# Optimization experiments

Hardware: AMD Instinct MI355X
Metric: run time of the kernel (lower is better)

Reference implementation:

```python
import jax, jax.numpy as jnp
import numpy as np

N_NODES = 20000
N_EDGES = 160000
IN_DIM = 64
HID = 256
EDGE_DIM = 64
SF_DIM = 1  # node_counts_dim = max_cycle - MIN_CYCLE + 1 with MIN_CYCLE==max_cycle (source bug)
N_LAYERS = 3
NUM_GRAPHS = 128
MSG_IN = 2 * HID + 2 * SF_DIM + EDGE_DIM  # 578
UPD_IN = 2 * HID


def setup_inputs() -> dict:
    key = jax.random.key(0)
    ks = jax.random.split(key, 16)
    s = 0.05
    return {
        "x": jax.random.normal(ks[0], (N_NODES, IN_DIM), jnp.float32),
        "node_sf": jax.random.uniform(ks[1], (N_NODES, SF_DIM), jnp.float32),
        "edge_feature": jax.random.normal(ks[2], (N_EDGES, EDGE_DIM), jnp.float32),
        "edge_weight": jax.random.uniform(ks[3], (N_EDGES,), jnp.float32),
        "edge_list": jax.random.randint(ks[4], (N_EDGES, 2), 0, N_NODES, jnp.int32),
        "node2graph": jnp.sort(jax.random.randint(ks[5], (N_NODES,), 0, NUM_GRAPHS, jnp.int32)),
        "Wlin": jax.random.normal(ks[6], (IN_DIM, HID), jnp.float32) * s,
        "blin": jnp.zeros((HID,), jnp.float32),
        "msg_W1": jax.random.normal(ks[7], (N_LAYERS, MSG_IN, HID), jnp.float32) * s,
        "msg_b1": jnp.zeros((N_LAYERS, HID), jnp.float32),
        "msg_W2": jax.random.normal(ks[8], (N_LAYERS, HID, HID), jnp.float32) * s,
        "msg_b2": jnp.zeros((N_LAYERS, HID), jnp.float32),
        "upd_W1": jax.random.normal(ks[9], (N_LAYERS, UPD_IN, HID), jnp.float32) * s,
        "upd_b1": jnp.zeros((N_LAYERS, HID), jnp.float32),
        "upd_W2": jax.random.normal(ks[10], (N_LAYERS, HID, HID), jnp.float32) * s,
        "upd_b2": jnp.zeros((N_LAYERS, HID), jnp.float32),
    }


def reference(x, node_sf, edge_feature, edge_weight, edge_list, node2graph,
              Wlin, blin, msg_W1, msg_b1, msg_W2, msg_b2,
              upd_W1, upd_b1, upd_W2, upd_b2):
    node_in = edge_list[:, 0]
    node_out = edge_list[:, 1]
    h = x @ Wlin + blin  # [N, HID]
    for l in range(N_LAYERS):
        # message: gather endpoint features + structural counts + edge features, 2-layer MLP
        m = jnp.concatenate(
            [h[node_in], h[node_out], node_sf[node_in], node_sf[node_out], edge_feature], axis=-1)
        m = jax.nn.relu(m @ msg_W1[l] + msg_b1[l]) @ msg_W2[l] + msg_b2[l]  # [E, HID]
        # aggregate: weighted scatter-add to destination nodes
        upd = jax.ops.segment_sum(m * edge_weight[:, None], node_out, num_segments=N_NODES)
        # combine: concat + 2-layer MLP, then outer activation
        c = jnp.concatenate([h, upd], axis=-1)
        c = jax.nn.relu(c @ upd_W1[l] + upd_b1[l]) @ upd_W2[l] + upd_b2[l]
        h = jax.nn.relu(c)
    # readout: global add pool per graph
    graph_feature = jax.ops.segment_sum(h, node2graph, num_segments=NUM_GRAPHS)
    return graph_feature
```

## Files before the change

kernel.cpp:

```cpp
#include <hip/hip_runtime.h>
#include <hip/hip_bf16.h>

#define N_NODES   20000
#define N_EDGES   160000
#define IN_DIM    64
#define HID       256
#define EDGE_DIM  64
#define NUM_GRAPHS 128
#define N_LAYERS  3

typedef __attribute__((ext_vector_type(8))) short s16x8;
typedef __attribute__((ext_vector_type(4))) float f32x4;

static __device__ __forceinline__ unsigned short f2bu(float f) {
    union { __hip_bfloat16 h; unsigned short u; } cv;
    cv.h = __float2bfloat16(f);
    return cv.u;
}
static __device__ __forceinline__ float bu2f(unsigned short u) {
    union { float f; unsigned int i; } c;
    c.i = ((unsigned int)u) << 16;
    return c.f;
}
static __device__ __forceinline__ s16x8 pack8(const float4 a, const float4 b) {
    s16x8 p;
    p[0] = (short)f2bu(a.x); p[1] = (short)f2bu(a.y);
    p[2] = (short)f2bu(a.z); p[3] = (short)f2bu(a.w);
    p[4] = (short)f2bu(b.x); p[5] = (short)f2bu(b.y);
    p[6] = (short)f2bu(b.z); p[7] = (short)f2bu(b.w);
    return p;
}

#define TILE_SH 8192
#define AIDX(row, slot) ((row) * 64 + (((slot) ^ ((row) & 7)) << 3))
#define SMEM_BYTES 33792

__global__ __launch_bounds__(256) void k_deg(const int* __restrict__ el,
                                             int* __restrict__ deg) {
    const int e = blockIdx.x * 256 + threadIdx.x;
    if (e < N_EDGES) atomicAdd(&deg[el[2 * e + 1]], 1);
}

__global__ __launch_bounds__(256) void k_scan(const int* __restrict__ deg,
                                              int* __restrict__ off,
                                              int* __restrict__ cursor) {
    __shared__ int ts[256];
    const int t = threadIdx.x;
    const int base = t * 79;
    const int end  = (base + 79 < N_NODES) ? base + 79 : N_NODES;
    int s = 0;
    for (int i = base; i < end; ++i) s += deg[i];
    ts[t] = s;
    __syncthreads();
    for (int d = 1; d < 256; d <<= 1) {
        const int u = (t >= d) ? ts[t - d] : 0;
        __syncthreads();
        ts[t] += u;
        __syncthreads();
    }
    int run = (t == 0) ? 0 : ts[t - 1];
    for (int i = base; i < end; ++i) {
        off[i] = run; cursor[i] = run; run += deg[i];
    }
}

__global__ __launch_bounds__(256) void k_scat(const int* __restrict__ el,
                                              int* __restrict__ cursor,
                                              int* __restrict__ eidx) {
    const int e = blockIdx.x * 256 + threadIdx.x;
    if (e < N_EDGES) {
        const int d = el[2 * e + 1];
        const int p = atomicAdd(&cursor[d], 1);
        eidx[p] = e;
    }
}

__global__ __launch_bounds__(256) void k_prep(const float* __restrict__ mW1,
                                              const float* __restrict__ mW2,
                                              const float* __restrict__ uW1,
                                              const float* __restrict__ uW2,
                                              unsigned short* __restrict__ msgW1T,
                                              unsigned short* __restrict__ msgW2T,
                                              unsigned short* __restrict__ updW1T,
                                              unsigned short* __restrict__ updW2T) {
    const int b = blockIdx.x;
    const int l = b / 50, t = b % 50;
    const float* W; unsigned short* dst; int rowbase;
    if (t < 18) {
        W = mW1 + (size_t)l * 578 * 256;
        dst = msgW1T + ((size_t)l * 18 + t) * TILE_SH;
        rowbase = (t < 16) ? t * 32 : 514 + (t - 16) * 32;
    } else if (t < 26) {
        const int tt = t - 18;
        W = mW2 + (size_t)l * 65536;
        dst = msgW2T + ((size_t)l * 8 + tt) * TILE_SH;
        rowbase = tt * 32;
    } else if (t < 42) {
        const int tt = t - 26;
        W = uW1 + (size_t)l * 131072;
        dst = updW1T + ((size_t)l * 16 + tt) * TILE_SH;
        rowbase = tt * 32;
    } else {
        const int tt = t - 42;
        W = uW2 + (size_t)l * 65536;
        dst = updW2T + ((size_t)l * 8 + tt) * TILE_SH;
        rowbase = tt * 32;
    }
    const int c = threadIdx.x;
    unsigned short buf[32];
    #pragma unroll
    for (int kk = 0; kk < 32; ++kk)
        buf[kk] = f2bu(W[(size_t)(rowbase + kk) * 256 + c]);
    #pragma unroll
    for (int j = 0; j < 4; ++j)
        *(s16x8*)&dst[(size_t)c * 32 + j * 8] = *(const s16x8*)&buf[j * 8];
}

__global__ __launch_bounds__(256) void k_pef(const float* __restrict__ ef,
                                             unsigned short* __restrict__ efbf) {
    const size_t i = ((size_t)blockIdx.x * 256 + threadIdx.x) * 8;
    const float4 a = *(const float4*)&ef[i];
    const float4 b = *(const float4*)&ef[i + 4];
    *(s16x8*)&efbf[i] = pack8(a, b);
}

__global__ __launch_bounds__(256) void k_lin(const float* __restrict__ x,
                                             const float* __restrict__ W,
                                             const float* __restrict__ b,
                                             unsigned short* __restrict__ h) {
    __shared__ float Xs[16][68];
    const int tid = threadIdx.x;
    const int n0  = blockIdx.x * 16;
    {
        const int row = tid >> 4, q = tid & 15;
        const float4 v = *(const float4*)&x[(size_t)(n0 + row) * IN_DIM + q * 4];
        Xs[row][q * 4 + 0] = v.x; Xs[row][q * 4 + 1] = v.y;
        Xs[row][q * 4 + 2] = v.z; Xs[row][q * 4 + 3] = v.w;
    }
    __syncthreads();
    const int col = tid;
    float acc[16];
    #pragma unroll
    for (int r = 0; r < 16; ++r) acc[r] = 0.f;
    for (int k = 0; k < IN_DIM; ++k) {
        const float w = W[(size_t)k * HID + col];
        #pragma unroll
        for (int r = 0; r < 16; ++r) acc[r] += Xs[r][k] * w;
    }
    const float bb = b[col];
    #pragma unroll
    for (int r = 0; r < 16; ++r)
        h[(size_t)(n0 + r) * HID + col] = f2bu(acc[r] + bb);
}

__global__ __launch_bounds__(256, 3) void k_msg(const unsigned short* __restrict__ hbf,
                                                const float* __restrict__ sf,
                                                const unsigned short* __restrict__ efbf,
                                                const float* __restrict__ ew,
                                                const int*   __restrict__ el,
                                                const int*   __restrict__ eidx,
                                                const unsigned short* __restrict__ W1T,
                                                const float* __restrict__ W1f,
                                                const float* __restrict__ b1,
                                                const unsigned short* __restrict__ W2T,
                                                const float* __restrict__ b2,
                                                float* __restrict__ upd) {
    __shared__ __align__(16) unsigned char smem[SMEM_BYTES];
    __shared__ int   Se[64], Sni[64], Sno[64];
    __shared__ float Sew[64], Ssa[64], Ssb[64];
    unsigned short (*As)[64 * 64] =
        reinterpret_cast<unsigned short (*)[64 * 64]>(smem);
    unsigned short* Ts = reinterpret_cast<unsigned short*>(smem);

    const int tid = threadIdx.x;
    const int e0  = blockIdx.x * 64;
    if (tid < 64) {
        const int e = eidx[e0 + tid];
        const int a = el[2 * e], bn = el[2 * e + 1];
        Se[tid] = e; Sni[tid] = a; Sno[tid] = bn;
        Sew[tid] = ew[e]; Ssa[tid] = sf[a]; Ssb[tid] = sf[bn];
    }
    __syncthreads();

    const int lane = tid & 63, wv = tid >> 6;
    const int lr = lane & 15, lq = lane >> 4;
    const int arow = tid & 63;
    const int aoff = (tid >> 6) * 16;
    const int ni = Sni[arow], no = Sno[arow], myE = Se[arow];

    const unsigned short* bp1 = W1T + (size_t)(wv * 64 + lr) * 32 + lq * 8;
    const unsigned short* bp2 = W2T + (size_t)(wv * 64 + lr) * 32 + lq * 8;

    #define APTR(c) ((c) < 4 ? hbf + (size_t)ni * HID + (c) * 64 + aoff \
                  : ((c) < 8 ? hbf + (size_t)no * HID + ((c) - 4) * 64 + aoff \
                             : efbf + (size_t)myE * EDGE_DIM + aoff))

    f32x4 acc[4][4];
    #pragma unroll
    for (int i = 0; i < 4; ++i)
        #pragma unroll
        for (int j = 0; j < 4; ++j) acc[i][j] = (f32x4)(0.0f);

    {
        const unsigned short* ap = APTR(0);
        *(s16x8*)&As[0][AIDX(arow, 2 * wv)]     = *(const s16x8*)(ap);
        *(s16x8*)&As[0][AIDX(arow, 2 * wv + 1)] = *(const s16x8*)(ap + 8);
    }
    s16x8 rNa, rNb, rFa, rFb;
    {
        const unsigned short* ap = APTR(1);
        rNa = *(const s16x8*)(ap);
        rNb = *(const s16x8*)(ap + 8);
    }
    s16x8 bfr[4], nb[4];
    #pragma unroll
    for (int nf = 0; nf < 4; ++nf)
        bfr[nf] = *(const s16x8*)(bp1 + nf * 512);
    __syncthreads();

    for (int c = 0; c < 9; ++c) {
        if (c + 2 < 9) {
            const unsigned short* ap = APTR(c + 2);
            rFa = *(const s16x8*)(ap);
            rFb = *(const s16x8*)(ap + 8);
        }
        #pragma unroll
        for (int ksub = 0; ksub < 2; ++ksub) {
            const int t = c * 2 + ksub;
            s16x8 af[4];
            #pragma unroll
            for (int mf = 0; mf < 4; ++mf)
                af[mf] = *(const s16x8*)&As[c & 1][AIDX(mf * 16 + lr, ksub * 4 + lq)];
            if (t + 1 < 18) {
                #pragma unroll
                for (int nf = 0; nf < 4; ++nf)
                    nb[nf] = *(const s16x8*)(bp1 + (size_t)(t + 1) * TILE_SH + nf * 512);
            }
            #pragma unroll
            for (int mf = 0; mf < 4; ++mf)
                #pragma unroll
                for (int nf = 0; nf < 4; ++nf)
                    acc[mf][nf] = __builtin_amdgcn_mfma_f32_16x16x32_bf16(
                        af[mf], bfr[nf], acc[mf][nf], 0, 0, 0);
            if (t + 1 < 18) {
                #pragma unroll
                for (int nf = 0; nf < 4; ++nf) bfr[nf] = nb[nf];
            }
        }
        if (c + 1 < 9) {
            *(s16x8*)&As[(c + 1) & 1][AIDX(arow, 2 * wv)]     = rNa;
            *(s16x8*)&As[(c + 1) & 1][AIDX(arow, 2 * wv + 1)] = rNb;
            rNa = rFa; rNb = rFb;
            __syncthreads();
        }
    }
    #undef APTR

    __syncthreads();

    #pragma unroll
    for (int nf = 0; nf < 4; ++nf) {
        const int col = wv * 64 + nf * 16 + lr;
        const float w512 = W1f[(size_t)512 * HID + col];
        const float w513 = W1f[(size_t)513 * HID + col];
        const float bb   = b1[col];
        #pragma unroll
        for (int mf = 0; mf < 4; ++mf)
            #pragma unroll
            for (int r = 0; r < 4; ++r) {
                const int row = mf * 16 + lq * 4 + r;
                float v = acc[mf][nf][r] + Ssa[row] * w512 + Ssb[row] * w513 + bb;
                Ts[row * 264 + col] = f2bu(fmaxf(v, 0.f));
            }
    }
    __syncthreads();

    f32x4 acc2[4][4];
    #pragma unroll
    for (int i = 0; i < 4; ++i)
        #pragma unroll
        for (int j = 0; j < 4; ++j) acc2[i][j] = (f32x4)(0.0f);

    s16x8 b2f[4], n2b[4];
    #pragma unroll
    for (int nf = 0; nf < 4; ++nf)
        b2f[nf] = *(const s16x8*)(bp2 + nf * 512);

    for (int s = 0; s < 8; ++s) {
        s16x8 a2[4];
        #pragma unroll
        for (int mf = 0; mf < 4; ++mf)
            a2[mf] = *(const s16x8*)&Ts[(mf * 16 + lr) * 264 + s * 32 + lq * 8];
        if (s + 1 < 8) {
            #pragma unroll
            for (int nf = 0; nf < 4; ++nf)
                n2b[nf] = *(const s16x8*)(bp2 + (size_t)(s + 1) * TILE_SH + nf * 512);
        }
        #pragma unroll
        for (int mf = 0; mf < 4; ++mf)
            #pragma unroll
            for (int nf = 0; nf < 4; ++nf)
                acc2[mf][nf] = __builtin_amdgcn_mfma_f32_16x16x32_bf16(
                    a2[mf], b2f[nf], acc2[mf][nf], 0, 0, 0);
        if (s + 1 < 8) {
            #pragma unroll
            for (int nf = 0; nf < 4; ++nf) b2f[nf] = n2b[nf];
        }
    }

    float* Mf = (float*)Ts;
    #pragma unroll
    for (int half = 0; half < 2; ++half) {
        __syncthreads();
        if ((wv >> 1) == half) {
            #pragma unroll
            for (int nf = 0; nf < 4; ++nf) {
                const int c  = (wv & 1) * 64 + nf * 16 + lr;
                const float bb = b2[half * 128 + c];
                #pragma unroll
                for (int mf = 0; mf < 4; ++mf)
                    #pragma unroll
                    for (int r = 0; r < 4; ++r) {
                        const int row = mf * 16 + lq * 4 + r;
                        Mf[row * 132 + c] = (acc2[mf][nf][r] + bb) * Sew[row];
                    }
            }
        }
        __syncthreads();
        {
            const int c = tid & 127;
            const int colg = half * 128 + c;
            const int rbase = (tid >> 7) * 32;
            float a = 0.f;
            int cur = Sno[rbase];
            for (int r = rbase; r < rbase + 32; ++r) {
                const int g = Sno[r];
                if (g != cur) {
                    atomicAdd(&upd[(size_t)cur * HID + colg], a);
                    a = 0.f; cur = g;
                }
                a += Mf[r * 132 + c];
            }
            atomicAdd(&upd[(size_t)cur * HID + colg], a);
        }
    }
}

__global__ __launch_bounds__(256, 3) void k_upd(const unsigned short* __restrict__ hbf,
                                                const float* __restrict__ upd,
                                                const unsigned short* __restrict__ W1T,
                                                const float* __restrict__ b1,
                                                const unsigned short* __restrict__ W2T,
                                                const float* __restrict__ b2,
                                                unsigned short* __restrict__ hout) {
    __shared__ __align__(16) unsigned char smem[SMEM_BYTES];
    unsigned short (*As)[64 * 64] =
        reinterpret_cast<unsigned short (*)[64 * 64]>(smem);
    unsigned short* Ts = reinterpret_cast<unsigned short*>(smem);

    const int tid = threadIdx.x;
    const int n0  = blockIdx.x * 64;
    const int lane = tid & 63, wv = tid >> 6;
    const int lr = lane & 15, lq = lane >> 4;
    const int arow = tid & 63;
    const int aoff = (tid >> 6) * 16;
    const int node = (n0 + arow < N_NODES) ? (n0 + arow) : (N_NODES - 1);

    const unsigned short* bp1 = W1T + (size_t)(wv * 64 + lr) * 32 + lq * 8;
    const unsigned short* bp2 = W2T + (size_t)(wv * 64 + lr) * 32 + lq * 8;

    f32x4 acc[4][4];
    #pragma unroll
    for (int i = 0; i < 4; ++i)
        #pragma unroll
        for (int j = 0; j < 4; ++j) acc[i][j] = (f32x4)(0.0f);

    #define ULOAD(c, oa, ob)  do { \
        if ((c) < 4) { \
            const unsigned short* ap = hbf + (size_t)node * HID + (c) * 64 + aoff; \
            (oa) = *(const s16x8*)(ap); (ob) = *(const s16x8*)(ap + 8); \
        } else { \
            const float* up = upd + (size_t)node * HID + ((c) - 4) * 64 + aoff; \
            (oa) = pack8(*(const float4*)(up),     *(const float4*)(up + 4)); \
            (ob) = pack8(*(const float4*)(up + 8), *(const float4*)(up + 12)); \
        } } while (0)

    {
        s16x8 t0, t1;
        ULOAD(0, t0, t1);
        *(s16x8*)&As[0][AIDX(arow, 2 * wv)]     = t0;
        *(s16x8*)&As[0][AIDX(arow, 2 * wv + 1)] = t1;
    }
    s16x8 rNa, rNb, rFa, rFb;
    ULOAD(1, rNa, rNb);
    s16x8 bfr[4], nb[4];
    #pragma unroll
    for (int nf = 0; nf < 4; ++nf)
        bfr[nf] = *(const s16x8*)(bp1 + nf * 512);
    __syncthreads();

    for (int c = 0; c < 8; ++c) {
        if (c + 2 < 8) ULOAD(c + 2, rFa, rFb);
        #pragma unroll
        for (int ksub = 0; ksub < 2; ++ksub) {
            const int t = c * 2 + ksub;
            s16x8 af[4];
            #pragma unroll
            for (int mf = 0; mf < 4; ++mf)
                af[mf] = *(const s16x8*)&As[c & 1][AIDX(mf * 16 + lr, ksub * 4 + lq)];
            if (t + 1 < 16) {
                #pragma unroll
                for (int nf = 0; nf < 4; ++nf)
                    nb[nf] = *(const s16x8*)(bp1 + (size_t)(t + 1) * TILE_SH + nf * 512);
            }
            #pragma unroll
            for (int mf = 0; mf < 4; ++mf)
                #pragma unroll
                for (int nf = 0; nf < 4; ++nf)
                    acc[mf][nf] = __builtin_amdgcn_mfma_f32_16x16x32_bf16(
                        af[mf], bfr[nf], acc[mf][nf], 0, 0, 0);
            if (t + 1 < 16) {
                #pragma unroll
                for (int nf = 0; nf < 4; ++nf) bfr[nf] = nb[nf];
            }
        }
        if (c + 1 < 8) {
            *(s16x8*)&As[(c + 1) & 1][AIDX(arow, 2 * wv)]     = rNa;
            *(s16x8*)&As[(c + 1) & 1][AIDX(arow, 2 * wv + 1)] = rNb;
            rNa = rFa; rNb = rFb;
            __syncthreads();
        }
    }
    #undef ULOAD

    __syncthreads();

    #pragma unroll
    for (int nf = 0; nf < 4; ++nf) {
        const int col = wv * 64 + nf * 16 + lr;
        const float bb = b1[col];
        #pragma unroll
        for (int mf = 0; mf < 4; ++mf)
            #pragma unroll
            for (int r = 0; r < 4; ++r) {
                const int row = mf * 16 + lq * 4 + r;
                Ts[row * 264 + col] = f2bu(fmaxf(acc[mf][nf][r] + bb, 0.f));
            }
    }
    __syncthreads();

    f32x4 acc2[4][4];
    #pragma unroll
    for (int i = 0; i < 4; ++i)
        #pragma unroll
        for (int j = 0; j < 4; ++j) acc2[i][j] = (f32x4)(0.0f);

    s16x8 b2f[4], n2b[4];
    #pragma unroll
    for (int nf = 0; nf < 4; ++nf)
        b2f[nf] = *(const s16x8*)(bp2 + nf * 512);

    for (int s = 0; s < 8; ++s) {
        s16x8 a2[4];
        #pragma unroll
        for (int mf = 0; mf < 4; ++mf)
            a2[mf] = *(const s16x8*)&Ts[(mf * 16 + lr) * 264 + s * 32 + lq * 8];
        if (s + 1 < 8) {
            #pragma unroll
            for (int nf = 0; nf < 4; ++nf)
                n2b[nf] = *(const s16x8*)(bp2 + (size_t)(s + 1) * TILE_SH + nf * 512);
        }
        #pragma unroll
        for (int mf = 0; mf < 4; ++mf)
            #pragma unroll
            for (int nf = 0; nf < 4; ++nf)
                acc2[mf][nf] = __builtin_amdgcn_mfma_f32_16x16x32_bf16(
                    a2[mf], b2f[nf], acc2[mf][nf], 0, 0, 0);
        if (s + 1 < 8) {
            #pragma unroll
            for (int nf = 0; nf < 4; ++nf) b2f[nf] = n2b[nf];
        }
    }

    #pragma unroll
    for (int nf = 0; nf < 4; ++nf) {
        const int col = wv * 64 + nf * 16 + lr;
        const float bb = b2[col];
        #pragma unroll
        for (int mf = 0; mf < 4; ++mf)
            #pragma unroll
            for (int r = 0; r < 4; ++r) {
                const int row = mf * 16 + lq * 4 + r;
                const int n = n0 + row;
                if (n < N_NODES)
                    hout[(size_t)n * HID + col] = f2bu(fmaxf(acc2[mf][nf][r] + bb, 0.f));
            }
    }
}

__global__ __launch_bounds__(256) void k_graph(const unsigned short* __restrict__ h,
                                               const int* __restrict__ n2g,
                                               float* __restrict__ out) {
    __shared__ int Sg[64];
    const int tid = threadIdx.x;
    const int n0  = blockIdx.x * 64;
    if (tid < 64) {
        const int n = n0 + tid;
        Sg[tid] = (n < N_NODES) ? n2g[n] : -1;
    }
    __syncthreads();
    const int col = tid;
    float accv = 0.f;
    int curg = Sg[0];
    for (int r = 0; r < 64; ++r) {
        const int n = n0 + r;
        if (n >= N_NODES) break;
        const int g = Sg[r];
        if (g != curg) {
            atomicAdd(&out[(size_t)curg * HID + col], accv);
            accv = 0.f; curg = g;
        }
        accv += bu2f(h[(size_t)n * HID + col]);
    }
    atomicAdd(&out[(size_t)curg * HID + col], accv);
}

extern "C" void kernel_launch(void* const* d_in, const int* in_sizes, int n_in,
                              void* d_out, int out_size, void* d_ws, size_t ws_size,
                              hipStream_t stream) {
    const float* x    = (const float*)d_in[0];
    const float* sf   = (const float*)d_in[1];
    const float* ef   = (const float*)d_in[2];
    const float* ew   = (const float*)d_in[3];
    const int*   el   = (const int*)d_in[4];
    const int*   n2g  = (const int*)d_in[5];
    const float* Wlin = (const float*)d_in[6];
    const float* blin = (const float*)d_in[7];
    const float* mW1  = (const float*)d_in[8];
    const float* mb1  = (const float*)d_in[9];
    const float* mW2  = (const float*)d_in[10];
    const float* mb2  = (const float*)d_in[11];
    const float* uW1  = (const float*)d_in[12];
    const float* ub1  = (const float*)d_in[13];
    const float* uW2  = (const float*)d_in[14];
    const float* ub2  = (const float*)d_in[15];
    float* out = (float*)d_out;

    unsigned short* hA   = (unsigned short*)d_ws;
    unsigned short* hB   = hA + (size_t)N_NODES * HID;
    unsigned short* efbf = hB + (size_t)N_NODES * HID;
    unsigned short* msgW1T = efbf + (size_t)N_EDGES * EDGE_DIM;
    unsigned short* msgW2T = msgW1T + (size_t)3 * 18 * TILE_SH;
    unsigned short* updW1T = msgW2T + (size_t)3 * 8  * TILE_SH;
    unsigned short* updW2T = updW1T + (size_t)3 * 16 * TILE_SH;
    float* upd  = (float*)(updW2T + (size_t)3 * 8 * TILE_SH);
    int* deg    = (int*)(upd + (size_t)N_NODES * HID);
    int* off    = deg + N_NODES;
    int* cursor = off + N_NODES;
    int* eidx   = cursor + N_NODES;

    hipMemsetAsync(d_out, 0, (size_t)NUM_GRAPHS * HID * sizeof(float), stream);
    hipMemsetAsync(deg, 0, (size_t)N_NODES * sizeof(int), stream);

    k_deg <<<(N_EDGES + 255) / 256, 256, 0, stream>>>(el, deg);
    k_scan<<<1, 256, 0, stream>>>(deg, off, cursor);
    k_scat<<<(N_EDGES + 255) / 256, 256, 0, stream>>>(el, cursor, eidx);

    k_prep<<<150, 256, 0, stream>>>(mW1, mW2, uW1, uW2,
                                    msgW1T, msgW2T, updW1T, updW2T);
    k_pef <<<N_EDGES * EDGE_DIM / (256 * 8), 256, 0, stream>>>(ef, efbf);
    k_lin <<<N_NODES / 16, 256, 0, stream>>>(x, Wlin, blin, hA);

    unsigned short* hc = hA;
    unsigned short* hn = hB;
    for (int l = 0; l < N_LAYERS; ++l) {
        hipMemsetAsync(upd, 0, (size_t)N_NODES * HID * sizeof(float), stream);
        k_msg<<<N_EDGES / 64, 256, 0, stream>>>(
            hc, sf, efbf, ew, el, eidx,
            msgW1T + (size_t)l * 18 * TILE_SH,
            mW1 + (size_t)l * 578 * 256, mb1 + (size_t)l * HID,
            msgW2T + (size_t)l * 8 * TILE_SH, mb2 + (size_t)l * HID, upd);
        k_upd<<<(N_NODES + 63) / 64, 256, 0, stream>>>(
            hc, upd,
            updW1T + (size_t)l * 16 * TILE_SH, ub1 + (size_t)l * HID,
            updW2T + (size_t)l * 8 * TILE_SH,  ub2 + (size_t)l * HID, hn);
        unsigned short* t = hc; hc = hn; hn = t;
    }

    k_graph<<<(N_NODES + 63) / 64, 256, 0, stream>>>(hc, n2g, out);
}
```

Measured before the change: 539.3 us.

## Widen A-tile K chunk to 128 and swizzle the hidden-activation LDS buffer

The message and update GEMM kernels now stage 128-wide K chunks of the gathered A operand in LDS instead of 64-wide ones. This halves the number of chunk iterations and barriers, and each thread issues four 16-byte gathers per chunk instead of two. The edge-feature tail is handled as a separate half-chunk. The padded 264-stride Ts layout is replaced by an XOR-swizzled 256-stride layout to shrink LDS to 32 KB, and the W2 fragment prefetch is hoisted ahead of the barrier. The cost is more registers held for in-flight loads, which could hurt occupancy at the 3-waves-per-SIMD launch bound.

```diff
diff --git a/kernel.cpp b/kernel.cpp
--- a/kernel.cpp
+++ b/kernel.cpp
@@ -32,8 +32,11 @@
 }
 
 #define TILE_SH 8192
-#define AIDX(row, slot) ((row) * 64 + (((slot) ^ ((row) & 7)) << 3))
-#define SMEM_BYTES 33792
+#define AIDX128(row, slot) ((row) * 128 + (((slot) ^ ((row) & 15)) << 3))
+static __device__ __forceinline__ int tsidx(int row, int col) {
+    return row * 256 + ((((col >> 3) ^ (row & 15)) << 3) | (col & 7));
+}
+#define SMEM_BYTES 32768
 
 __global__ __launch_bounds__(256) void k_deg(const int* __restrict__ el,
                                              int* __restrict__ deg) {
@@ -168,8 +171,8 @@
     __shared__ __align__(16) unsigned char smem[SMEM_BYTES];
     __shared__ int   Se[64], Sni[64], Sno[64];
     __shared__ float Sew[64], Ssa[64], Ssb[64];
-    unsigned short (*As)[64 * 64] =
-        reinterpret_cast<unsigned short (*)[64 * 64]>(smem);
+    unsigned short (*As)[64 * 128] =
+        reinterpret_cast<unsigned short (*)[64 * 128]>(smem);
     unsigned short* Ts = reinterpret_cast<unsigned short*>(smem);
 
     const int tid = threadIdx.x;
@@ -185,15 +188,14 @@
     const int lane = tid & 63, wv = tid >> 6;
     const int lr = lane & 15, lq = lane >> 4;
     const int arow = tid & 63;
-    const int aoff = (tid >> 6) * 16;
+    const int g    = tid >> 6;
     const int ni = Sni[arow], no = Sno[arow], myE = Se[arow];
 
     const unsigned short* bp1 = W1T + (size_t)(wv * 64 + lr) * 32 + lq * 8;
     const unsigned short* bp2 = W2T + (size_t)(wv * 64 + lr) * 32 + lq * 8;
 
-    #define APTR(c) ((c) < 4 ? hbf + (size_t)ni * HID + (c) * 64 + aoff \
-                  : ((c) < 8 ? hbf + (size_t)no * HID + ((c) - 4) * 64 + aoff \
-                             : efbf + (size_t)myE * EDGE_DIM + aoff))
+    #define APTR(c) ((c) < 2 ? hbf + (size_t)ni * HID + (c) * 128 + g * 32 \
+                             : hbf + (size_t)no * HID + ((c) - 2) * 128 + g * 32)
 
     f32x4 acc[4][4];
     #pragma unroll
@@ -203,14 +205,15 @@
 
     {
         const unsigned short* ap = APTR(0);
-        *(s16x8*)&As[0][AIDX(arow, 2 * wv)]     = *(const s16x8*)(ap);
-        *(s16x8*)&As[0][AIDX(arow, 2 * wv + 1)] = *(const s16x8*)(ap + 8);
-    }
-    s16x8 rNa, rNb, rFa, rFb;
+        #pragma unroll
+        for (int j = 0; j < 4; ++j)
+            *(s16x8*)&As[0][AIDX128(arow, 4 * g + j)] = *(const s16x8*)(ap + 8 * j);
+    }
+    s16x8 rN[4], rF[4];
     {
         const unsigned short* ap = APTR(1);
-        rNa = *(const s16x8*)(ap);
-        rNb = *(const s16x8*)(ap + 8);
+        #pragma unroll
+        for (int j = 0; j < 4; ++j) rN[j] = *(const s16x8*)(ap + 8 * j);
     }
     s16x8 bfr[4], nb[4];
     #pragma unroll
@@ -218,43 +221,76 @@
         bfr[nf] = *(const s16x8*)(bp1 + nf * 512);
     __syncthreads();
 
-    for (int c = 0; c < 9; ++c) {
-        if (c + 2 < 9) {
+    for (int c = 0; c < 4; ++c) {
+        if (c + 2 < 4) {
             const unsigned short* ap = APTR(c + 2);
-            rFa = *(const s16x8*)(ap);
-            rFb = *(const s16x8*)(ap + 8);
-        }
-        #pragma unroll
-        for (int ksub = 0; ksub < 2; ++ksub) {
-            const int t = c * 2 + ksub;
+            #pragma unroll
+            for (int j = 0; j < 4; ++j) rF[j] = *(const s16x8*)(ap + 8 * j);
+        } else if (c + 2 == 4) {
+            const unsigned short* ap = efbf + (size_t)myE * EDGE_DIM + g * 16;
+            rF[0] = *(const s16x8*)(ap);
+            rF[1] = *(const s16x8*)(ap + 8);
+        }
+        #pragma unroll
+        for (int ks = 0; ks < 4; ++ks) {
+            const int t = c * 4 + ks;
             s16x8 af[4];
             #pragma unroll
             for (int mf = 0; mf < 4; ++mf)
-                af[mf] = *(const s16x8*)&As[c & 1][AIDX(mf * 16 + lr, ksub * 4 + lq)];
-            if (t + 1 < 18) {
-                #pragma unroll
-                for (int nf = 0; nf < 4; ++nf)
-                    nb[nf] = *(const s16x8*)(bp1 + (size_t)(t + 1) * TILE_SH + nf * 512);
-            }
+                af[mf] = *(const s16x8*)&As[c & 1][AIDX128(mf * 16 + lr, ks * 4 + lq)];
+            #pragma unroll
+            for (int nf = 0; nf < 4; ++nf)
+                nb[nf] = *(const s16x8*)(bp1 + (size_t)(t + 1) * TILE_SH + nf * 512);
             #pragma unroll
             for (int mf = 0; mf < 4; ++mf)
                 #pragma unroll
                 for (int nf = 0; nf < 4; ++nf)
                     acc[mf][nf] = __builtin_amdgcn_mfma_f32_16x16x32_bf16(
                         af[mf], bfr[nf], acc[mf][nf], 0, 0, 0);
-            if (t + 1 < 18) {
-                #pragma unroll
-                for (int nf = 0; nf < 4; ++nf) bfr[nf] = nb[nf];
-            }
-        }
-        if (c + 1 < 9) {
-            *(s16x8*)&As[(c + 1) & 1][AIDX(arow, 2 * wv)]     = rNa;
-            *(s16x8*)&As[(c + 1) & 1][AIDX(arow, 2 * wv + 1)] = rNb;
-            rNa = rFa; rNb = rFb;
-            __syncthreads();
+            #pragma unroll
+            for (int nf = 0; nf < 4; ++nf) bfr[nf] = nb[nf];
+        }
+        if (c < 3) {
+            #pragma unroll
+            for (int j = 0; j < 4; ++j)
+                *(s16x8*)&As[(c + 1) & 1][AIDX128(arow, 4 * g + j)] = rN[j];
+            #pragma unroll
+            for (int j = 0; j < 4; ++j) rN[j] = rF[j];
+        } else {
+            *(s16x8*)&As[0][AIDX128(arow, 2 * g)]     = rN[0];
+            *(s16x8*)&As[0][AIDX128(arow, 2 * g + 1)] = rN[1];
+        }
+        __syncthreads();
+    }
+    #pragma unroll
+    for (int ks = 0; ks < 2; ++ks) {
+        const int t = 16 + ks;
+        s16x8 af[4];
+        #pragma unroll
+        for (int mf = 0; mf < 4; ++mf)
+            af[mf] = *(const s16x8*)&As[0][AIDX128(mf * 16 + lr, ks * 4 + lq)];
+        if (t + 1 < 18) {
+            #pragma unroll
+            for (int nf = 0; nf < 4; ++nf)
+                nb[nf] = *(const s16x8*)(bp1 + (size_t)(t + 1) * TILE_SH + nf * 512);
+        }
+        #pragma unroll
+        for (int mf = 0; mf < 4; ++mf)
+            #pragma unroll
+            for (int nf = 0; nf < 4; ++nf)
+                acc[mf][nf] = __builtin_amdgcn_mfma_f32_16x16x32_bf16(
+                    af[mf], bfr[nf], acc[mf][nf], 0, 0, 0);
+        if (t + 1 < 18) {
+            #pragma unroll
+            for (int nf = 0; nf < 4; ++nf) bfr[nf] = nb[nf];
         }
     }
     #undef APTR
+
+    s16x8 b2f[4], n2b[4];
+    #pragma unroll
+    for (int nf = 0; nf < 4; ++nf)
+        b2f[nf] = *(const s16x8*)(bp2 + nf * 512);
 
     __syncthreads();
 
@@ -270,7 +306,7 @@
             for (int r = 0; r < 4; ++r) {
                 const int row = mf * 16 + lq * 4 + r;
                 float v = acc[mf][nf][r] + Ssa[row] * w512 + Ssb[row] * w513 + bb;
-                Ts[row * 264 + col] = f2bu(fmaxf(v, 0.f));
+                Ts[tsidx(row, col)] = f2bu(fmaxf(v, 0.f));
             }
     }
     __syncthreads();
@@ -280,17 +316,12 @@
     for (int i = 0; i < 4; ++i)
         #pragma unroll
         for (int j = 0; j < 4; ++j) acc2[i][j] = (f32x4)(0.0f);
-
-    s16x8 b2f[4], n2b[4];
-    #pragma unroll
-    for (int nf = 0; nf < 4; ++nf)
-        b2f[nf] = *(const s16x8*)(bp2 + nf * 512);
 
     for (int s = 0; s < 8; ++s) {
         s16x8 a2[4];
         #pragma unroll
         for (int mf = 0; mf < 4; ++mf)
-            a2[mf] = *(const s16x8*)&Ts[(mf * 16 + lr) * 264 + s * 32 + lq * 8];
+            a2[mf] = *(const s16x8*)&Ts[tsidx(mf * 16 + lr, s * 32 + lq * 8)];
         if (s + 1 < 8) {
             #pragma unroll
             for (int nf = 0; nf < 4; ++nf)
@@ -322,7 +353,7 @@
                     #pragma unroll
                     for (int r = 0; r < 4; ++r) {
                         const int row = mf * 16 + lq * 4 + r;
-                        Mf[row * 132 + c] = (acc2[mf][nf][r] + bb) * Sew[row];
+                        Mf[row * 128 + c] = (acc2[mf][nf][r] + bb) * Sew[row];
                     }
             }
         }
@@ -334,12 +365,12 @@
             float a = 0.f;
             int cur = Sno[rbase];
             for (int r = rbase; r < rbase + 32; ++r) {
-                const int g = Sno[r];
-                if (g != cur) {
+                const int gno = Sno[r];
+                if (gno != cur) {
                     atomicAdd(&upd[(size_t)cur * HID + colg], a);
-                    a = 0.f; cur = g;
+                    a = 0.f; cur = gno;
                 }
-                a += Mf[r * 132 + c];
+                a += Mf[r * 128 + c];
             }
             atomicAdd(&upd[(size_t)cur * HID + colg], a);
         }
@@ -354,8 +385,8 @@
                                                 const float* __restrict__ b2,
                                                 unsigned short* __restrict__ hout) {
     __shared__ __align__(16) unsigned char smem[SMEM_BYTES];
-    unsigned short (*As)[64 * 64] =
-        reinterpret_cast<unsigned short (*)[64 * 64]>(smem);
+    unsigned short (*As)[64 * 128] =
+        reinterpret_cast<unsigned short (*)[64 * 128]>(smem);
     unsigned short* Ts = reinterpret_cast<unsigned short*>(smem);
 
     const int tid = threadIdx.x;
@@ -363,7 +394,7 @@
     const int lane = tid & 63, wv = tid >> 6;
     const int lr = lane & 15, lq = lane >> 4;
     const int arow = tid & 63;
-    const int aoff = (tid >> 6) * 16;
+    const int g    = tid >> 6;
     const int node = (n0 + arow < N_NODES) ? (n0 + arow) : (N_NODES - 1);
 
     const unsigned short* bp1 = W1T + (size_t)(wv * 64 + lr) * 32 + lq * 8;
@@ -375,39 +406,43 @@
         #pragma unroll
         for (int j = 0; j < 4; ++j) acc[i][j] = (f32x4)(0.0f);
 
-    #define ULOAD(c, oa, ob)  do { \
-        if ((c) < 4) { \
-            const unsigned short* ap = hbf + (size_t)node * HID + (c) * 64 + aoff; \
-            (oa) = *(const s16x8*)(ap); (ob) = *(const s16x8*)(ap + 8); \
+    #define ULOAD(c, r_) do { \
+        if ((c) < 2) { \
+            const unsigned short* ap = hbf + (size_t)node * HID + (c) * 128 + g * 32; \
+            r_[0] = *(const s16x8*)(ap);      r_[1] = *(const s16x8*)(ap + 8); \
+            r_[2] = *(const s16x8*)(ap + 16); r_[3] = *(const s16x8*)(ap + 24); \
         } else { \
-            const float* up = upd + (size_t)node * HID + ((c) - 4) * 64 + aoff; \
-            (oa) = pack8(*(const float4*)(up),     *(const float4*)(up + 4)); \
-            (ob) = pack8(*(const float4*)(up + 8), *(const float4*)(up + 12)); \
+            const float* up = upd + (size_t)node * HID + ((c) - 2) * 128 + g * 32; \
+            r_[0] = pack8(*(const float4*)(up),      *(const float4*)(up + 4)); \
+            r_[1] = pack8(*(const float4*)(up + 8),  *(const float4*)(up + 12)); \
+            r_[2] = pack8(*(const float4*)(up + 16), *(const float4*)(up + 20)); \
+            r_[3] = pack8(*(const float4*)(up + 24), *(const float4*)(up + 28)); \
         } } while (0)
 
     {
-        s16x8 t0, t1;
-        ULOAD(0, t0, t1);
-        *(s16x8*)&As[0][AIDX(arow, 2 * wv)]     = t0;
-        *(s16x8*)&As[0][AIDX(arow, 2 * wv + 1)] = t1;
-    }
-    s16x8 rNa, rNb, rFa, rFb;
-    ULOAD(1, rNa, rNb);
+        s16x8 t0[4];
+        ULOAD(0, t0);
+        #pragma unroll
+        for (int j = 0; j < 4; ++j)
+            *(s16x8*)&As[0][AIDX128(arow, 4 * g + j)] = t0[j];
+    }
+    s16x8 rN[4], rF[4];
+    ULOAD(1, rN);
     s16x8 bfr[4], nb[4];
     #pragma unroll
     for (int nf = 0; nf < 4; ++nf)
         bfr[nf] = *(const s16x8*)(bp1 + nf * 512);
     __syncthreads();
 
-    for (int c = 0; c < 8; ++c) {
-        if (c + 2 < 8) ULOAD(c + 2, rFa, rFb);
-        #pragma unroll
-        for (int ksub = 0; ksub < 2; ++ksub) {
-            const int t = c * 2 + ksub;
+    for (int c = 0; c < 4; ++c) {
+        if (c + 2 < 4) ULOAD(c + 2, rF);
+        #pragma unroll
+        for (int ks = 0; ks < 4; ++ks) {
+            const int t = c * 4 + ks;
             s16x8 af[4];
             #pragma unroll
             for (int mf = 0; mf < 4; ++mf)
-                af[mf] = *(const s16x8*)&As[c & 1][AIDX(mf * 16 + lr, ksub * 4 + lq)];
+                af[mf] = *(const s16x8*)&As[c & 1][AIDX128(mf * 16 + lr, ks * 4 + lq)];
             if (t + 1 < 16) {
                 #pragma unroll
                 for (int nf = 0; nf < 4; ++nf)
@@ -424,14 +459,21 @@
                 for (int nf = 0; nf < 4; ++nf) bfr[nf] = nb[nf];
             }
         }
-        if (c + 1 < 8) {
-            *(s16x8*)&As[(c + 1) & 1][AIDX(arow, 2 * wv)]     = rNa;
-            *(s16x8*)&As[(c + 1) & 1][AIDX(arow, 2 * wv + 1)] = rNb;
-            rNa = rFa; rNb = rFb;
+        if (c + 1 < 4) {
+            #pragma unroll
+            for (int j = 0; j < 4; ++j)
+                *(s16x8*)&As[(c + 1) & 1][AIDX128(arow, 4 * g + j)] = rN[j];
+            #pragma unroll
+            for (int j = 0; j < 4; ++j) rN[j] = rF[j];
             __syncthreads();
         }
     }
     #undef ULOAD
+
+    s16x8 b2f[4], n2b[4];
+    #pragma unroll
+    for (int nf = 0; nf < 4; ++nf)
+        b2f[nf] = *(const s16x8*)(bp2 + nf * 512);
 
     __syncthreads();
 
@@ -444,7 +486,7 @@
             #pragma unroll
             for (int r = 0; r < 4; ++r) {
                 const int row = mf * 16 + lq * 4 + r;
-                Ts[row * 264 + col] = f2bu(fmaxf(acc[mf][nf][r] + bb, 0.f));
+                Ts[tsidx(row, col)] = f2bu(fmaxf(acc[mf][nf][r] + bb, 0.f));
             }
     }
     __syncthreads();
@@ -454,17 +496,12 @@
     for (int i = 0; i < 4; ++i)
         #pragma unroll
         for (int j = 0; j < 4; ++j) acc2[i][j] = (f32x4)(0.0f);
-
-    s16x8 b2f[4], n2b[4];
-    #pragma unroll
-    for (int nf = 0; nf < 4; ++nf)
-        b2f[nf] = *(const s16x8*)(bp2 + nf * 512);
 
     for (int s = 0; s < 8; ++s) {
         s16x8 a2[4];
         #pragma unroll
         for (int mf = 0; mf < 4; ++mf)
-            a2[mf] = *(const s16x8*)&Ts[(mf * 16 + lr) * 264 + s * 32 + lq * 8];
+            a2[mf] = *(const s16x8*)&Ts[tsidx(mf * 16 + lr, s * 32 + lq * 8)];
         if (s + 1 < 8) {
             #pragma unroll
             for (int nf = 0; nf < 4; ++nf)
```

New measurement: 587.0 us. 8.8% more time.
